# Kernel optimization log

Hardware: AMD Instinct MI355X
Metric: run time of the kernel (lower is better)

The kernel has to match this reference:

```python
import jax, jax.numpy as jnp
import numpy as np

B, T, N = 1024, 64, 128
E = 256          # embedding_size
H = 256          # hidden_size (== attention embed_dim)
NH = 256         # node_hidden_size (kdim/vdim)
HEADS = 4
DH = H // HEADS
F = 1            # edge_feature_len
L = 2            # gru layers


def setup_inputs() -> dict:
    key = jax.random.key(0)
    ks = iter(jax.random.split(key, 40))

    def rn(shape, s=0.05):
        return jax.random.normal(next(ks), shape, dtype=jnp.float32) * s

    z = lambda *shape: jnp.zeros(shape, jnp.float32)
    inp = {
        "x": rn((B, T, F), 1.0),
        "prev_node_hiddens": rn((B, N, NH), 1.0),
        # set_first_layer_hidden: layer 0 from GraphLevelRNN, layers > 0 zeroed
        "h0": jnp.concatenate([rn((1, B, H), 1.0), jnp.zeros((L - 1, B, H), jnp.float32)], axis=0),
        "W_in": rn((E, F)), "b_in": z(E),
        "gru_Wih0": rn((3 * H, E)), "gru_Whh0": rn((3 * H, H)),
        "gru_bih0": z(3 * H), "gru_bhh0": z(3 * H),
        "gru_Wih1": rn((3 * H, H)), "gru_Whh1": rn((3 * H, H)),
        "gru_bih1": z(3 * H), "gru_bhh1": z(3 * H),
        "Wq": rn((H, H)), "Wk": rn((H, NH)), "Wv": rn((H, NH)),
        "bq": z(H), "bk": z(H), "bv": z(H),
        "Wo": rn((H, H)), "bo": z(H),
        "Wc": rn((E, 2 * H)), "bc": z(E),
        "W1": rn((E, E)), "b1": z(E),
        "W2": rn((F, E)), "b2": z(F),
        "attn_mask": jnp.zeros((B, N), dtype=bool),
    }
    return inp


def _gru_cell(x, h, Wih, Whh, bih, bhh):
    # PyTorch GRU cell math
    gi = x @ Wih.T + bih
    gh = h @ Whh.T + bhh
    i_r, i_z, i_n = jnp.split(gi, 3, axis=-1)
    h_r, h_z, h_n = jnp.split(gh, 3, axis=-1)
    r = jax.nn.sigmoid(i_r + h_r)
    zg = jax.nn.sigmoid(i_z + h_z)
    n = jnp.tanh(i_n + r * h_n)
    return (1.0 - zg) * n + zg * h


def reference(x, prev_node_hiddens, h0, W_in, b_in,
              gru_Wih0, gru_Whh0, gru_bih0, gru_bhh0,
              gru_Wih1, gru_Whh1, gru_bih1, gru_bhh1,
              Wq, Wk, Wv, bq, bk, bv, Wo, bo,
              Wc, bc, W1, b1, W2, b2, attn_mask):
    emb = jax.nn.relu(x @ W_in.T + b_in)                       # [B,T,E]
    # K/V projections depend only on prev_node_hiddens; project once
    # (math identical to the per-step nn.MultiheadAttention call).
    k = (prev_node_hiddens @ Wk.T + bk).reshape(B, N, HEADS, DH)
    v = (prev_node_hiddens @ Wv.T + bv).reshape(B, N, HEADS, DH)
    scale = 1.0 / np.sqrt(DH).astype(np.float32)
    neg = jnp.asarray(-1e9, jnp.float32)
    mask = attn_mask[:, None, :]                               # [B,1,N]

    def step(carry, xt):
        h_prev0, h_prev1 = carry
        h0n = _gru_cell(xt, h_prev0, gru_Wih0, gru_Whh0, gru_bih0, gru_bhh0)
        h1n = _gru_cell(h0n, h_prev1, gru_Wih1, gru_Whh1, gru_bih1, gru_bhh1)
        # single-token query = last-layer hidden state
        q = ((h1n @ Wq.T + bq) * scale).reshape(B, HEADS, DH)
        scores = jnp.einsum('bhd,bnhd->bhn', q, k)             # [B,HEADS,N]
        scores = jnp.where(mask, neg, scores)
        a = jax.nn.softmax(scores, axis=-1)
        ctx = jnp.einsum('bhn,bnhd->bhd', a, v).reshape(B, H) @ Wo.T + bo
        comb = jax.nn.relu(jnp.concatenate([h1n, ctx], axis=-1) @ Wc.T + bc)
        out = jax.nn.relu(comb @ W1.T + b1) @ W2.T + b2        # [B,F]
        return (h0n, h1n), out

    _, outs = jax.lax.scan(step, (h0[0], h0[1]), jnp.swapaxes(emb, 0, 1))
    logits = jnp.swapaxes(outs, 0, 1)                          # [B,T,F]
    return jax.nn.sigmoid(logits)
```

## Files before the change

### kernel.cpp

```cpp
#include <hip/hip_runtime.h>
#include <hip/hip_bf16.h>
#include <cstddef>
#include <cstdint>


#define B_  1024
#define T_  64
#define N_  128

typedef __attribute__((ext_vector_type(8))) short s16x8;
typedef __attribute__((ext_vector_type(4))) float f32x4;

__device__ __forceinline__ unsigned short f2b(float f) {
  unsigned int u = __float_as_uint(f);
  u += 0x7FFFu + ((u >> 16) & 1u);
  return (unsigned short)(u >> 16);
}
__device__ __forceinline__ float b2f(unsigned short s){ return __uint_as_float(((unsigned int)s) << 16); }
__device__ __forceinline__ float sigmoidf_(float x){ return 1.0f / (1.0f + __expf(-x)); }
__device__ __forceinline__ float tanhf_(float x){
  float t = __expf(-2.0f * fabsf(x));
  float r = (1.0f - t) / (1.0f + t);
  return x >= 0.0f ? r : -r;
}
__device__ __forceinline__ void gld_lds16(const void* g, void* l) {
  __builtin_amdgcn_global_load_lds(
      (const __attribute__((address_space(1))) void*)g,
      (__attribute__((address_space(3))) void*)l, 16, 0, 0);
}
#define WAITV3 asm volatile("s_waitcnt vmcnt(3)" ::: "memory")
#define WAITV0 asm volatile("s_waitcnt vmcnt(0)" ::: "memory")

__global__ void cvt_bf16(const float* __restrict__ s, unsigned short* __restrict__ d, int n) {
  int i = blockIdx.x * blockDim.x + threadIdx.x;
  if (i < n) d[i] = f2b(s[i]);
}

#define LDA 264
#define LDB 40

__global__ __launch_bounds__(256) void kv_gemm(
    const float* __restrict__ phn,
    const float* __restrict__ Wk, const float* __restrict__ Wv,
    const float* __restrict__ bk, const float* __restrict__ bv,
    unsigned short* __restrict__ k_all, unsigned short* __restrict__ v_all)
{
  __shared__ __align__(16) unsigned short Alds[64 * LDA];
  __shared__ __align__(16) unsigned short Blds[256 * LDB];
  const int tid = threadIdx.x;
  const int m0 = blockIdx.x * 64;
  const int n0 = blockIdx.y * 256;
  #pragma unroll
  for (int p = 0; p < 16; ++p) {
    int q = p * 256 + tid;
    int row = q >> 6, kq = q & 63;
    float4 f = *(const float4*)&phn[(size_t)(m0 + row) * 256 + (size_t)kq * 4];
    ushort4 h; h.x = f2b(f.x); h.y = f2b(f.y); h.z = f2b(f.z); h.w = f2b(f.w);
    *(ushort4*)&Alds[row * LDA + kq * 4] = h;
  }
  const int wave = tid >> 6, lane = tid & 63;
  const int lr = lane & 15, lk = (lane >> 4) * 8;
  f32x4 acc[16];
  #pragma unroll
  for (int t = 0; t < 16; ++t) {
    int j = n0 + t * 16 + lr;
    float bz = (j < 256) ? bk[j] : bv[j - 256];
    acc[t][0] = bz; acc[t][1] = bz; acc[t][2] = bz; acc[t][3] = bz;
  }
  for (int kc = 0; kc < 8; ++kc) {
    __syncthreads();
    #pragma unroll
    for (int p = 0; p < 8; ++p) {
      int j = p * 32 + (tid >> 3);
      int jg = n0 + j;
      const float* wrow = (jg < 256) ? &Wk[(size_t)jg * 256] : &Wv[(size_t)(jg - 256) * 256];
      float4 f = *(const float4*)&wrow[kc * 32 + (tid & 7) * 4];
      ushort4 h; h.x = f2b(f.x); h.y = f2b(f.y); h.z = f2b(f.z); h.w = f2b(f.w);
      *(ushort4*)&Blds[j * LDB + (tid & 7) * 4] = h;
    }
    __syncthreads();
    s16x8 a = *(const s16x8*)&Alds[(wave * 16 + lr) * LDA + kc * 32 + lk];
    #pragma unroll
    for (int t = 0; t < 16; ++t) {
      s16x8 b = *(const s16x8*)&Blds[(t * 16 + lr) * LDB + lk];
      acc[t] = __builtin_amdgcn_mfma_f32_16x16x32_bf16(a, b, acc[t], 0, 0, 0);
    }
  }
  const int rbase = m0 + wave * 16 + (lane >> 4) * 4;
  #pragma unroll
  for (int t = 0; t < 16; ++t) {
    int j = n0 + t * 16 + lr;
    #pragma unroll
    for (int i = 0; i < 4; ++i) {
      size_t m = (size_t)(rbase + i);
      unsigned short hv = f2b(acc[t][i]);
      if (j < 256) k_all[m * 256 + j] = hv;
      else         v_all[m * 256 + (j - 256)] = hv;
    }
  }
}

__global__ __launch_bounds__(256) void gi0_gemm(
    const float* __restrict__ x, const float* __restrict__ W_in, const float* __restrict__ b_in,
    const float* __restrict__ Wih0, const float* __restrict__ bih0,
    unsigned short* __restrict__ gi0)
{
  __shared__ __align__(16) unsigned short Alds[64 * LDA];
  __shared__ __align__(16) unsigned short Blds[256 * LDB];
  const int tid = threadIdx.x;
  const int m0 = blockIdx.x * 64;
  const int f0 = blockIdx.y * 256;
  float win = W_in[tid], bin = b_in[tid];
  for (int p = 0; p < 64; ++p) {
    float e = fmaxf(fmaf(x[m0 + p], win, bin), 0.0f);
    Alds[p * LDA + tid] = f2b(e);
  }
  const int wave = tid >> 6, lane = tid & 63;
  const int lr = lane & 15, lk = (lane >> 4) * 8;
  f32x4 acc[16];
  #pragma unroll
  for (int t = 0; t < 16; ++t) {
    float bz = bih0[f0 + t * 16 + lr];
    acc[t][0] = bz; acc[t][1] = bz; acc[t][2] = bz; acc[t][3] = bz;
  }
  for (int kc = 0; kc < 8; ++kc) {
    __syncthreads();
    #pragma unroll
    for (int p = 0; p < 8; ++p) {
      int j = p * 32 + (tid >> 3);
      const float* wrow = &Wih0[(size_t)(f0 + j) * 256];
      float4 f = *(const float4*)&wrow[kc * 32 + (tid & 7) * 4];
      ushort4 h; h.x = f2b(f.x); h.y = f2b(f.y); h.z = f2b(f.z); h.w = f2b(f.w);
      *(ushort4*)&Blds[j * LDB + (tid & 7) * 4] = h;
    }
    __syncthreads();
    s16x8 a = *(const s16x8*)&Alds[(wave * 16 + lr) * LDA + kc * 32 + lk];
    #pragma unroll
    for (int t = 0; t < 16; ++t) {
      s16x8 b = *(const s16x8*)&Blds[(t * 16 + lr) * LDB + lk];
      acc[t] = __builtin_amdgcn_mfma_f32_16x16x32_bf16(a, b, acc[t], 0, 0, 0);
    }
  }
  const int rbase = m0 + wave * 16 + (lane >> 4) * 4;
  #pragma unroll
  for (int t = 0; t < 16; ++t) {
    int f = f0 + t * 16 + lr;
    #pragma unroll
    for (int i = 0; i < 4; ++i) {
      int m = rbase + i;
      gi0[((size_t)(m & 63) * 1024 + (m >> 6)) * 768 + f] = f2b(acc[t][i]);
    }
  }
}

__global__ __launch_bounds__(512) void seq2_kernel(
    const unsigned short* __restrict__ gi0,
    const float* __restrict__ h0_init,
    const unsigned short* __restrict__ w_hh0, const float* __restrict__ bhh0,
    const unsigned short* __restrict__ w_ih1, const float* __restrict__ bih1,
    const unsigned short* __restrict__ w_hh1, const float* __restrict__ bhh1,
    unsigned short* __restrict__ h1_all)
{
  __shared__ __align__(16) unsigned short wbuf[8][8][512];
  __shared__ __align__(16) float h0f[4][256];
  __shared__ __align__(16) float h1f[4][256];
  __shared__ __align__(16) unsigned short h0b[4][264];
  __shared__ __align__(16) unsigned short h1b[4][264];

  const int tid = threadIdx.x;
  const int w = tid >> 6, lane = tid & 63;
  const int col = lane & 15, kg = lane >> 4;
  const int b0 = blockIdx.x * 4;

  for (int i = tid; i < 1024; i += 512) {
    int g = i >> 8, f = i & 255;
    float v0 = h0_init[(size_t)(b0 + g) * 256 + f];
    float v1 = h0_init[(size_t)(B_ * 256) + (size_t)(b0 + g) * 256 + f];
    h0f[g][f] = v0; h1f[g][f] = v1;
    h0b[g][f] = f2b(v0); h1b[g][f] = f2b(v1);
  }
  __syncthreads();

  unsigned int off6[6];
  #pragma unroll
  for (int j = 0; j < 6; ++j) {
    int r0 = (j >> 1) * 256 + w * 32 + (j & 1) * 16;
    off6[j] = (unsigned)((r0 + col) * 256 + kg * 8);
  }
  float bb0[6], bb1[12];
  #pragma unroll
  for (int j = 0; j < 6; ++j) {
    int f = (j >> 1) * 256 + w * 32 + (j & 1) * 16 + col;
    bb0[j] = bhh0[f];
    bb1[j] = bih1[f];
    bb1[6 + j] = bhh1[f];
  }

  #pragma unroll 1
  for (int t = 0; t < T_; ++t) {
    f32x4 acc[6];
    #pragma unroll
    for (int j = 0; j < 6; ++j) { float bz = bb0[j]; acc[j][0]=bz; acc[j][1]=bz; acc[j][2]=bz; acc[j][3]=bz; }
    #pragma unroll
    for (int kc = 0; kc < 4; ++kc)
      gld_lds16(w_hh0 + off6[0] + kc * 32, &wbuf[w][kc][0]);
    #pragma unroll
    for (int j = 0; j < 6; ++j) {
      #pragma unroll
      for (int kc = 0; kc < 8; ++kc) {
        const int g = j * 8 + kc;
        if (g < 44) { WAITV3; } else if (g == 44) { WAITV0; }
        s16x8 bf_ = *(const s16x8*)&wbuf[w][g & 7][(size_t)lane * 8];
        s16x8 af_ = *(const s16x8*)&h0b[col & 3][kc * 32 + kg * 8];
        acc[j] = __builtin_amdgcn_mfma_f32_16x16x32_bf16(af_, bf_, acc[j], 0, 0, 0);
        if (g + 4 < 48) {
          const int gn = g + 4, jn = gn >> 3, kn = gn & 7;
          gld_lds16(w_hh0 + off6[jn] + kn * 32, &wbuf[w][gn & 7][0]);
        }
      }
    }
    if (lane < 16) {
      const size_t gbase = ((size_t)t * 1024 + b0) * 768;
      #pragma unroll
      for (int i = 0; i < 4; ++i) {
        const unsigned short* gp = gi0 + gbase + (size_t)i * 768;
        #pragma unroll
        for (int sub = 0; sub < 2; ++sub) {
          int f = w * 32 + sub * 16 + col;
          float ir = b2f(gp[f]), iz = b2f(gp[256 + f]), in_ = b2f(gp[512 + f]);
          float r = sigmoidf_(ir + acc[sub][i]);
          float z = sigmoidf_(iz + acc[2 + sub][i]);
          float n = tanhf_(in_ + r * acc[4 + sub][i]);
          float hn = (1.0f - z) * n + z * h0f[i][f];
          h0f[i][f] = hn;
          h0b[i][f] = f2b(hn);
        }
      }
    }
    __syncthreads();

    f32x4 acc2[12];
    #pragma unroll
    for (int j = 0; j < 12; ++j) { float bz = bb1[j]; acc2[j][0]=bz; acc2[j][1]=bz; acc2[j][2]=bz; acc2[j][3]=bz; }
    #pragma unroll
    for (int kc = 0; kc < 4; ++kc)
      gld_lds16(w_ih1 + off6[0] + kc * 32, &wbuf[w][kc][0]);
    #pragma unroll
    for (int j = 0; j < 12; ++j) {
      #pragma unroll
      for (int kc = 0; kc < 8; ++kc) {
        const int g = j * 8 + kc;
        if (g < 92) { WAITV3; } else if (g == 92) { WAITV0; }
        s16x8 bf_ = *(const s16x8*)&wbuf[w][g & 7][(size_t)lane * 8];
        s16x8 af_;
        if (j < 6) af_ = *(const s16x8*)&h0b[col & 3][kc * 32 + kg * 8];
        else       af_ = *(const s16x8*)&h1b[col & 3][kc * 32 + kg * 8];
        acc2[j] = __builtin_amdgcn_mfma_f32_16x16x32_bf16(af_, bf_, acc2[j], 0, 0, 0);
        if (g + 4 < 96) {
          const int gn = g + 4, jn = gn >> 3, kn = gn & 7;
          const unsigned short* wb = (jn < 6) ? w_ih1 : w_hh1;
          const unsigned int of = (jn < 6) ? off6[jn] : off6[jn - 6];
          gld_lds16(wb + of + kn * 32, &wbuf[w][gn & 7][0]);
        }
      }
    }
    if (lane < 16) {
      #pragma unroll
      for (int i = 0; i < 4; ++i) {
        #pragma unroll
        for (int sub = 0; sub < 2; ++sub) {
          int f = w * 32 + sub * 16 + col;
          float r = sigmoidf_(acc2[sub][i] + acc2[6 + sub][i]);
          float z = sigmoidf_(acc2[2 + sub][i] + acc2[8 + sub][i]);
          float n = tanhf_(acc2[4 + sub][i] + r * acc2[10 + sub][i]);
          float hn = (1.0f - z) * n + z * h1f[i][f];
          h1f[i][f] = hn;
          unsigned short hb = f2b(hn);
          h1b[i][f] = hb;
          h1_all[((size_t)(b0 + i) * T_ + t) * 256 + f] = hb;
        }
      }
    }
    __syncthreads();
  }
}

__global__ __launch_bounds__(256) void q_gemm(
    const unsigned short* __restrict__ h1_all,
    const unsigned short* __restrict__ w_q, const float* __restrict__ bq,
    unsigned short* __restrict__ q_all)
{
  __shared__ __align__(16) unsigned short A[64][264];
  const int tid = threadIdx.x;
  const int m0 = blockIdx.x * 64;
  #pragma unroll
  for (int p = 0; p < 8; ++p) {
    int idx = p * 256 + tid;
    int row = idx >> 5, c8 = idx & 31;
    *(uint4*)&A[row][c8 * 8] = *(const uint4*)&h1_all[(size_t)(m0 + row) * 256 + c8 * 8];
  }
  __syncthreads();
  const int wv = tid >> 6, lane = tid & 63;
  const int col = lane & 15, kg = lane >> 4;
  f32x4 acc[16];
  #pragma unroll
  for (int ct = 0; ct < 16; ++ct) {
    float bz = bq[ct * 16 + col];
    acc[ct][0]=bz; acc[ct][1]=bz; acc[ct][2]=bz; acc[ct][3]=bz;
  }
  #pragma unroll
  for (int kc = 0; kc < 8; ++kc) {
    s16x8 af = *(const s16x8*)&A[wv * 16 + col][kc * 32 + kg * 8];
    #pragma unroll
    for (int ct = 0; ct < 16; ++ct) {
      s16x8 bf = *(const s16x8*)&w_q[(size_t)(ct * 16 + col) * 256 + kc * 32 + kg * 8];
      acc[ct] = __builtin_amdgcn_mfma_f32_16x16x32_bf16(af, bf, acc[ct], 0, 0, 0);
    }
  }
  const int r0 = m0 + wv * 16 + kg * 4;
  #pragma unroll
  for (int ct = 0; ct < 16; ++ct) {
    int j = ct * 16 + col;
    #pragma unroll
    for (int i = 0; i < 4; ++i)
      q_all[(size_t)(r0 + i) * 256 + j] = f2b(acc[ct][i] * 0.125f);
  }
}

__global__ __launch_bounds__(256) void attn_kernel(
    const unsigned short* __restrict__ q_all,
    const unsigned short* __restrict__ k_all,
    const unsigned short* __restrict__ v_all,
    const unsigned char* __restrict__ amask,
    unsigned short* __restrict__ ctx_all)
{
  __shared__ __align__(16) unsigned short qh[64][72];
  __shared__ __align__(16) unsigned short kh[128][72];
  __shared__ __align__(16) unsigned short vT[64][136];
  __shared__ __align__(16) unsigned short P[64][136];
  const int b = blockIdx.x;
  const int tid = threadIdx.x;
  const int wv = tid >> 6, lane = tid & 63;
  const int col = lane & 15, kg = lane >> 4;
  bool mk[8];
  #pragma unroll
  for (int nt = 0; nt < 8; ++nt) mk[nt] = amask[(size_t)b * 128 + nt * 16 + col] != 0;

  #pragma unroll 1
  for (int h = 0; h < 4; ++h) {
    #pragma unroll
    for (int p = 0; p < 2; ++p) {
      int idx = p * 256 + tid, row = idx >> 3, c8 = idx & 7;
      *(uint4*)&qh[row][c8 * 8] = *(const uint4*)&q_all[((size_t)b * 64 + row) * 256 + h * 64 + c8 * 8];
    }
    #pragma unroll
    for (int p = 0; p < 4; ++p) {
      int idx = p * 256 + tid, row = idx >> 3, c8 = idx & 7;
      *(uint4*)&kh[row][c8 * 8] = *(const uint4*)&k_all[((size_t)b * 128 + row) * 256 + h * 64 + c8 * 8];
    }
    #pragma unroll
    for (int rep = 0; rep < 32; ++rep) {
      int e = rep * 256 + tid;
      int n = e >> 6, d = e & 63;
      vT[d][n] = v_all[((size_t)b * 128 + n) * 256 + h * 64 + d];
    }
    __syncthreads();

    s16x8 aq0 = *(const s16x8*)&qh[wv * 16 + col][kg * 8];
    s16x8 aq1 = *(const s16x8*)&qh[wv * 16 + col][32 + kg * 8];
    f32x4 s[8];
    #pragma unroll
    for (int nt = 0; nt < 8; ++nt) {
      f32x4 z = {0.f, 0.f, 0.f, 0.f};
      s16x8 bk0 = *(const s16x8*)&kh[nt * 16 + col][kg * 8];
      s16x8 bk1 = *(const s16x8*)&kh[nt * 16 + col][32 + kg * 8];
      z = __builtin_amdgcn_mfma_f32_16x16x32_bf16(aq0, bk0, z, 0, 0, 0);
      z = __builtin_amdgcn_mfma_f32_16x16x32_bf16(aq1, bk1, z, 0, 0, 0);
      s[nt] = z;
    }
    #pragma unroll
    for (int nt = 0; nt < 8; ++nt)
      if (mk[nt]) { s[nt][0] = -1e9f; s[nt][1] = -1e9f; s[nt][2] = -1e9f; s[nt][3] = -1e9f; }
    f32x4 mx = s[0];
    #pragma unroll
    for (int nt = 1; nt < 8; ++nt)
      #pragma unroll
      for (int i = 0; i < 4; ++i) mx[i] = fmaxf(mx[i], s[nt][i]);
    #pragma unroll
    for (int i = 0; i < 4; ++i) {
      float m = mx[i];
      m = fmaxf(m, __shfl_xor(m, 1)); m = fmaxf(m, __shfl_xor(m, 2));
      m = fmaxf(m, __shfl_xor(m, 4)); m = fmaxf(m, __shfl_xor(m, 8));
      mx[i] = m;
    }
    f32x4 sm = {0.f, 0.f, 0.f, 0.f};
    #pragma unroll
    for (int nt = 0; nt < 8; ++nt)
      #pragma unroll
      for (int i = 0; i < 4; ++i) { s[nt][i] = __expf(s[nt][i] - mx[i]); sm[i] += s[nt][i]; }
    #pragma unroll
    for (int i = 0; i < 4; ++i) {
      float t2 = sm[i];
      t2 += __shfl_xor(t2, 1); t2 += __shfl_xor(t2, 2);
      t2 += __shfl_xor(t2, 4); t2 += __shfl_xor(t2, 8);
      sm[i] = 1.0f / t2;
    }
    #pragma unroll
    for (int nt = 0; nt < 8; ++nt)
      #pragma unroll
      for (int i = 0; i < 4; ++i)
        P[wv * 16 + kg * 4 + i][nt * 16 + col] = f2b(s[nt][i] * sm[i]);
    __syncthreads();

    f32x4 c4[4];
    #pragma unroll
    for (int dt = 0; dt < 4; ++dt) { c4[dt][0]=0.f; c4[dt][1]=0.f; c4[dt][2]=0.f; c4[dt][3]=0.f; }
    #pragma unroll
    for (int kc = 0; kc < 4; ++kc) {
      s16x8 ap = *(const s16x8*)&P[wv * 16 + col][kc * 32 + kg * 8];
      #pragma unroll
      for (int dt = 0; dt < 4; ++dt) {
        s16x8 bv_ = *(const s16x8*)&vT[dt * 16 + col][kc * 32 + kg * 8];
        c4[dt] = __builtin_amdgcn_mfma_f32_16x16x32_bf16(ap, bv_, c4[dt], 0, 0, 0);
      }
    }
    #pragma unroll
    for (int dt = 0; dt < 4; ++dt) {
      int d = h * 64 + dt * 16 + col;
      #pragma unroll
      for (int i = 0; i < 4; ++i)
        ctx_all[((size_t)b * 64 + wv * 16 + kg * 4 + i) * 256 + d] = f2b(c4[dt][i]);
    }
    __syncthreads();
  }
}

__global__ __launch_bounds__(256) void out_chain(
    const unsigned short* __restrict__ h1_all,
    const unsigned short* __restrict__ ctx_all,
    const unsigned short* __restrict__ w_o, const float* __restrict__ bo,
    const unsigned short* __restrict__ w_c, const float* __restrict__ bc,
    const unsigned short* __restrict__ w_1, const float* __restrict__ b1,
    const float* __restrict__ W2, const float* __restrict__ b2,
    float* __restrict__ out)
{
  __shared__ __align__(16) unsigned short BufA[64][264];
  __shared__ __align__(16) unsigned short BufB[64][264];
  const int b = blockIdx.x;
  const int tid = threadIdx.x;
  const int wv = tid >> 6, lane = tid & 63;
  const int col = lane & 15, kg = lane >> 4;
  const size_t mbase = (size_t)b * 64;
  #pragma unroll
  for (int p = 0; p < 8; ++p) {
    int idx = p * 256 + tid, row = idx >> 5, c8 = idx & 31;
    *(uint4*)&BufA[row][c8 * 8] = *(const uint4*)&h1_all[(mbase + row) * 256 + c8 * 8];
    *(uint4*)&BufB[row][c8 * 8] = *(const uint4*)&ctx_all[(mbase + row) * 256 + c8 * 8];
  }
  __syncthreads();
  f32x4 acc[16];

  #pragma unroll
  for (int ct = 0; ct < 16; ++ct) { float bz = bo[ct*16+col]; acc[ct][0]=bz; acc[ct][1]=bz; acc[ct][2]=bz; acc[ct][3]=bz; }
  #pragma unroll
  for (int kc = 0; kc < 8; ++kc) {
    s16x8 af = *(const s16x8*)&BufB[wv * 16 + col][kc * 32 + kg * 8];
    #pragma unroll
    for (int ct = 0; ct < 16; ++ct) {
      s16x8 bf = *(const s16x8*)&w_o[(size_t)(ct * 16 + col) * 256 + kc * 32 + kg * 8];
      acc[ct] = __builtin_amdgcn_mfma_f32_16x16x32_bf16(af, bf, acc[ct], 0, 0, 0);
    }
  }
  __syncthreads();
  #pragma unroll
  for (int ct = 0; ct < 16; ++ct)
    #pragma unroll
    for (int i = 0; i < 4; ++i)
      BufB[wv * 16 + kg * 4 + i][ct * 16 + col] = f2b(acc[ct][i]);
  __syncthreads();

  #pragma unroll
  for (int ct = 0; ct < 16; ++ct) { float bz = bc[ct*16+col]; acc[ct][0]=bz; acc[ct][1]=bz; acc[ct][2]=bz; acc[ct][3]=bz; }
  #pragma unroll
  for (int kc = 0; kc < 16; ++kc) {
    s16x8 af;
    if (kc < 8) af = *(const s16x8*)&BufA[wv * 16 + col][kc * 32 + kg * 8];
    else        af = *(const s16x8*)&BufB[wv * 16 + col][(kc - 8) * 32 + kg * 8];
    #pragma unroll
    for (int ct = 0; ct < 16; ++ct) {
      s16x8 bf = *(const s16x8*)&w_c[(size_t)(ct * 16 + col) * 512 + kc * 32 + kg * 8];
      acc[ct] = __builtin_amdgcn_mfma_f32_16x16x32_bf16(af, bf, acc[ct], 0, 0, 0);
    }
  }
  __syncthreads();
  #pragma unroll
  for (int ct = 0; ct < 16; ++ct)
    #pragma unroll
    for (int i = 0; i < 4; ++i)
      BufB[wv * 16 + kg * 4 + i][ct * 16 + col] = f2b(fmaxf(acc[ct][i], 0.0f));
  __syncthreads();

  #pragma unroll
  for (int ct = 0; ct < 16; ++ct) { float bz = b1[ct*16+col]; acc[ct][0]=bz; acc[ct][1]=bz; acc[ct][2]=bz; acc[ct][3]=bz; }
  #pragma unroll
  for (int kc = 0; kc < 8; ++kc) {
    s16x8 af = *(const s16x8*)&BufB[wv * 16 + col][kc * 32 + kg * 8];
    #pragma unroll
    for (int ct = 0; ct < 16; ++ct) {
      s16x8 bf = *(const s16x8*)&w_1[(size_t)(ct * 16 + col) * 256 + kc * 32 + kg * 8];
      acc[ct] = __builtin_amdgcn_mfma_f32_16x16x32_bf16(af, bf, acc[ct], 0, 0, 0);
    }
  }
  __syncthreads();
  #pragma unroll
  for (int ct = 0; ct < 16; ++ct)
    #pragma unroll
    for (int i = 0; i < 4; ++i)
      BufA[wv * 16 + kg * 4 + i][ct * 16 + col] = f2b(fmaxf(acc[ct][i], 0.0f));
  __syncthreads();

  {
    int r = tid >> 2, qq = tid & 3;
    float a = 0.0f;
    #pragma unroll
    for (int i2 = 0; i2 < 64; ++i2) {
      int k = qq * 64 + i2;
      a += b2f(BufA[r][k]) * W2[k];
    }
    a += __shfl_xor(a, 1); a += __shfl_xor(a, 2);
    if (qq == 0) out[mbase + r] = sigmoidf_(a + b2[0]);
  }
}

extern "C" void kernel_launch(void* const* d_in, const int* in_sizes, int n_in,
                              void* d_out, int out_size, void* d_ws, size_t ws_size,
                              hipStream_t stream)
{
  (void)in_sizes; (void)n_in; (void)out_size;
  const float* x    = (const float*)d_in[0];
  const float* phn  = (const float*)d_in[1];
  const float* h0i  = (const float*)d_in[2];
  const float* W_in = (const float*)d_in[3];
  const float* b_in = (const float*)d_in[4];
  const float* Wih0 = (const float*)d_in[5];
  const float* Whh0 = (const float*)d_in[6];
  const float* bih0 = (const float*)d_in[7];
  const float* bhh0 = (const float*)d_in[8];
  const float* Wih1 = (const float*)d_in[9];
  const float* Whh1 = (const float*)d_in[10];
  const float* bih1 = (const float*)d_in[11];
  const float* bhh1 = (const float*)d_in[12];
  const float* Wq = (const float*)d_in[13];
  const float* Wk = (const float*)d_in[14];
  const float* Wv = (const float*)d_in[15];
  const float* bq = (const float*)d_in[16];
  const float* bk = (const float*)d_in[17];
  const float* bv = (const float*)d_in[18];
  const float* Wo = (const float*)d_in[19];
  const float* bo = (const float*)d_in[20];
  const float* Wc = (const float*)d_in[21];
  const float* bc = (const float*)d_in[22];
  const float* W1 = (const float*)d_in[23];
  const float* b1 = (const float*)d_in[24];
  const float* W2 = (const float*)d_in[25];
  const float* b2 = (const float*)d_in[26];
  const unsigned char* amask = (const unsigned char*)d_in[27];
  float* out = (float*)d_out;

  unsigned short* ws = (unsigned short*)d_ws;
  size_t off = 0;
  unsigned short* w_hh0 = ws + off; off += 196608;
  unsigned short* w_ih1 = ws + off; off += 196608;
  unsigned short* w_hh1 = ws + off; off += 196608;
  unsigned short* w_q   = ws + off; off += 65536;
  unsigned short* w_o   = ws + off; off += 65536;
  unsigned short* w_c   = ws + off; off += 131072;
  unsigned short* w_1   = ws + off; off += 65536;
  unsigned short* k_all = ws + off; off += (size_t)B_ * N_ * 256;
  unsigned short* v_all = ws + off; off += (size_t)B_ * N_ * 256;
  unsigned short* h1_all = ws + off; off += (size_t)B_ * T_ * 256;
  unsigned short* bigR  = ws + off; off += (size_t)B_ * T_ * 768;
  unsigned short* gi0   = bigR;
  unsigned short* q_all = bigR;
  unsigned short* ctx_all = bigR + (size_t)B_ * T_ * 256;
  if (ws_size < off * sizeof(unsigned short)) return;

  hipLaunchKernelGGL(cvt_bf16, dim3(384), dim3(512), 0, stream, Whh0, w_hh0, 196608);
  hipLaunchKernelGGL(cvt_bf16, dim3(384), dim3(512), 0, stream, Wih1, w_ih1, 196608);
  hipLaunchKernelGGL(cvt_bf16, dim3(384), dim3(512), 0, stream, Whh1, w_hh1, 196608);
  hipLaunchKernelGGL(cvt_bf16, dim3(128), dim3(512), 0, stream, Wq, w_q, 65536);
  hipLaunchKernelGGL(cvt_bf16, dim3(128), dim3(512), 0, stream, Wo, w_o, 65536);
  hipLaunchKernelGGL(cvt_bf16, dim3(256), dim3(512), 0, stream, Wc, w_c, 131072);
  hipLaunchKernelGGL(cvt_bf16, dim3(128), dim3(512), 0, stream, W1, w_1, 65536);

  hipLaunchKernelGGL(kv_gemm, dim3(2048, 2), dim3(256), 0, stream,
                     phn, Wk, Wv, bk, bv, k_all, v_all);
  hipLaunchKernelGGL(gi0_gemm, dim3(1024, 3), dim3(256), 0, stream,
                     x, W_in, b_in, Wih0, bih0, gi0);
  hipLaunchKernelGGL(seq2_kernel, dim3(256), dim3(512), 0, stream,
                     gi0, h0i, w_hh0, bhh0, w_ih1, bih1, w_hh1, bhh1, h1_all);
  hipLaunchKernelGGL(q_gemm, dim3(1024), dim3(256), 0, stream,
                     h1_all, w_q, bq, q_all);
  hipLaunchKernelGGL(attn_kernel, dim3(1024), dim3(256), 0, stream,
                     q_all, k_all, v_all, amask, ctx_all);
  hipLaunchKernelGGL(out_chain, dim3(1024), dim3(256), 0, stream,
                     h1_all, ctx_all, w_o, bo, w_c, bc, w_1, b1, W2, b2, out);
}
```

Baseline: 4.512 ms.

## Repack GRU weights into MFMA fragment order and batch 16 rows per block

Weights for the two recurrent GRU layers are pre-packed into per-wave, per-lane MFMA fragment order. The sequential kernel then streams them straight into registers with a software prefetch ring, replacing the LDS staging. Each block now handles 16 batch rows instead of 4, so every weight load feeds four times as many rows and all 16 MFMA rows do useful work. gi0 is async-loaded into LDS, hidden state stays in registers, and h1 is written back with vector stores. The grid shrinks to 64 blocks, which leaves most CUs idle and adds register pressure.

```diff
diff --git a/kernel.cpp b/kernel.cpp
--- a/kernel.cpp
+++ b/kernel.cpp
@@ -28,12 +28,32 @@
       (const __attribute__((address_space(1))) void*)g,
       (__attribute__((address_space(3))) void*)l, 16, 0, 0);
 }
-#define WAITV3 asm volatile("s_waitcnt vmcnt(3)" ::: "memory")
-#define WAITV0 asm volatile("s_waitcnt vmcnt(0)" ::: "memory")
 
 __global__ void cvt_bf16(const float* __restrict__ s, unsigned short* __restrict__ d, int n) {
   int i = blockIdx.x * blockDim.x + threadIdx.x;
   if (i < n) d[i] = f2b(s[i]);
+}
+
+__global__ void pack_w1(const float* __restrict__ Whh0, unsigned short* __restrict__ dst) {
+  int d = blockIdx.x * 256 + threadIdx.x;
+  int e = d & 7, l = (d >> 3) & 63, blk = d >> 9;
+  int kc = blk & 7, tj = blk >> 3;
+  int j = tj % 6, w = tj / 6;
+  int row = (j >> 1) * 256 + w * 32 + (j & 1) * 16 + (l & 15);
+  int colk = kc * 32 + (l >> 4) * 8 + e;
+  dst[d] = f2b(Whh0[(size_t)row * 256 + colk]);
+}
+__global__ void pack_w2(const float* __restrict__ Wih1, const float* __restrict__ Whh1,
+                        unsigned short* __restrict__ dst) {
+  int d = blockIdx.x * 256 + threadIdx.x;
+  int e = d & 7, l = (d >> 3) & 63, blk = d >> 9;
+  int kc = blk & 7, tj = blk >> 3;
+  int j = tj % 12, w = tj / 12;
+  int jj = (j < 6) ? j : j - 6;
+  int row = (jj >> 1) * 256 + w * 32 + (jj & 1) * 16 + (l & 15);
+  int colk = kc * 32 + (l >> 4) * 8 + e;
+  const float* src = (j < 6) ? Wih1 : Whh1;
+  dst[d] = f2b(src[(size_t)row * 256 + colk]);
 }
 
 #define LDA 264
@@ -153,40 +173,35 @@
   }
 }
 
-__global__ __launch_bounds__(512) void seq2_kernel(
+__global__ __launch_bounds__(512) void seq3_kernel(
     const unsigned short* __restrict__ gi0,
     const float* __restrict__ h0_init,
-    const unsigned short* __restrict__ w_hh0, const float* __restrict__ bhh0,
-    const unsigned short* __restrict__ w_ih1, const float* __restrict__ bih1,
-    const unsigned short* __restrict__ w_hh1, const float* __restrict__ bhh1,
+    const unsigned short* __restrict__ wpk1,
+    const float* __restrict__ bhh0,
+    const unsigned short* __restrict__ wpk2,
+    const float* __restrict__ bih1, const float* __restrict__ bhh1,
     unsigned short* __restrict__ h1_all)
 {
-  __shared__ __align__(16) unsigned short wbuf[8][8][512];
-  __shared__ __align__(16) float h0f[4][256];
-  __shared__ __align__(16) float h1f[4][256];
-  __shared__ __align__(16) unsigned short h0b[4][264];
-  __shared__ __align__(16) unsigned short h1b[4][264];
+  __shared__ __align__(16) unsigned short h0b[16][264];
+  __shared__ __align__(16) unsigned short h1b[16][264];
+  __shared__ __align__(16) unsigned short gi0s[16 * 768];
 
   const int tid = threadIdx.x;
   const int w = tid >> 6, lane = tid & 63;
   const int col = lane & 15, kg = lane >> 4;
-  const int b0 = blockIdx.x * 4;
-
-  for (int i = tid; i < 1024; i += 512) {
-    int g = i >> 8, f = i & 255;
-    float v0 = h0_init[(size_t)(b0 + g) * 256 + f];
-    float v1 = h0_init[(size_t)(B_ * 256) + (size_t)(b0 + g) * 256 + f];
-    h0f[g][f] = v0; h1f[g][f] = v1;
-    h0b[g][f] = f2b(v0); h1b[g][f] = f2b(v1);
-  }
-  __syncthreads();
-
-  unsigned int off6[6];
-  #pragma unroll
-  for (int j = 0; j < 6; ++j) {
-    int r0 = (j >> 1) * 256 + w * 32 + (j & 1) * 16;
-    off6[j] = (unsigned)((r0 + col) * 256 + kg * 8);
-  }
+  const int b0 = blockIdx.x * 16;
+
+  float hp0[8], hp1[8];
+  #pragma unroll
+  for (int sub = 0; sub < 2; ++sub)
+    #pragma unroll
+    for (int i = 0; i < 4; ++i) {
+      int bt = kg * 4 + i, fl = w * 32 + sub * 16 + col;
+      float v0 = h0_init[(size_t)(b0 + bt) * 256 + fl];
+      float v1 = h0_init[(size_t)(B_ * 256) + (size_t)(b0 + bt) * 256 + fl];
+      hp0[sub * 4 + i] = v0; hp1[sub * 4 + i] = v1;
+      h0b[bt][fl] = f2b(v0); h1b[bt][fl] = f2b(v1);
+    }
   float bb0[6], bb1[12];
   #pragma unroll
   for (int j = 0; j < 6; ++j) {
@@ -195,93 +210,105 @@
     bb1[j] = bih1[f];
     bb1[6 + j] = bhh1[f];
   }
+  __syncthreads();
+
+  const unsigned short* w1base = wpk1 + (size_t)w * 24576 + (size_t)lane * 8;
+  const unsigned short* w2base = wpk2 + (size_t)w * 49152 + (size_t)lane * 8;
+
+  s16x8 Wr[8];
 
   #pragma unroll 1
   for (int t = 0; t < T_; ++t) {
+    {
+      const unsigned short* gsrc = gi0 + ((size_t)t * 1024 + b0) * 768;
+      #pragma unroll
+      for (int c = 0; c < 3; ++c)
+        gld_lds16(gsrc + (size_t)(w * 3 + c) * 512 + (size_t)lane * 8,
+                  &gi0s[(w * 3 + c) * 512]);
+    }
+    __builtin_amdgcn_sched_barrier(0);
+    #pragma unroll
+    for (int p = 0; p < 6; ++p)
+      Wr[p] = *(const s16x8*)(w1base + (size_t)p * 512);
+    s16x8 h0o[8], h1o[8];
+    #pragma unroll
+    for (int kc = 0; kc < 8; ++kc) {
+      h0o[kc] = *(const s16x8*)&h0b[col][kc * 32 + kg * 8];
+      h1o[kc] = *(const s16x8*)&h1b[col][kc * 32 + kg * 8];
+    }
+    asm volatile("s_waitcnt vmcnt(6)" ::: "memory");
+    __syncthreads();
+
     f32x4 acc[6];
     #pragma unroll
     for (int j = 0; j < 6; ++j) { float bz = bb0[j]; acc[j][0]=bz; acc[j][1]=bz; acc[j][2]=bz; acc[j][3]=bz; }
-    #pragma unroll
-    for (int kc = 0; kc < 4; ++kc)
-      gld_lds16(w_hh0 + off6[0] + kc * 32, &wbuf[w][kc][0]);
     #pragma unroll
     for (int j = 0; j < 6; ++j) {
       #pragma unroll
       for (int kc = 0; kc < 8; ++kc) {
         const int g = j * 8 + kc;
-        if (g < 44) { WAITV3; } else if (g == 44) { WAITV0; }
-        s16x8 bf_ = *(const s16x8*)&wbuf[w][g & 7][(size_t)lane * 8];
-        s16x8 af_ = *(const s16x8*)&h0b[col & 3][kc * 32 + kg * 8];
-        acc[j] = __builtin_amdgcn_mfma_f32_16x16x32_bf16(af_, bf_, acc[j], 0, 0, 0);
-        if (g + 4 < 48) {
-          const int gn = g + 4, jn = gn >> 3, kn = gn & 7;
-          gld_lds16(w_hh0 + off6[jn] + kn * 32, &wbuf[w][gn & 7][0]);
-        }
+        if (g + 6 < 48) Wr[(g + 6) & 7] = *(const s16x8*)(w1base + (size_t)(g + 6) * 512);
+        else            Wr[(g + 6) & 7] = *(const s16x8*)(w2base + (size_t)(g + 6 - 48) * 512);
+        acc[j] = __builtin_amdgcn_mfma_f32_16x16x32_bf16(h0o[kc], Wr[g & 7], acc[j], 0, 0, 0);
       }
     }
-    if (lane < 16) {
-      const size_t gbase = ((size_t)t * 1024 + b0) * 768;
+    #pragma unroll
+    for (int sub = 0; sub < 2; ++sub) {
+      const int fl = w * 32 + sub * 16 + col;
       #pragma unroll
       for (int i = 0; i < 4; ++i) {
-        const unsigned short* gp = gi0 + gbase + (size_t)i * 768;
-        #pragma unroll
-        for (int sub = 0; sub < 2; ++sub) {
-          int f = w * 32 + sub * 16 + col;
-          float ir = b2f(gp[f]), iz = b2f(gp[256 + f]), in_ = b2f(gp[512 + f]);
-          float r = sigmoidf_(ir + acc[sub][i]);
-          float z = sigmoidf_(iz + acc[2 + sub][i]);
-          float n = tanhf_(in_ + r * acc[4 + sub][i]);
-          float hn = (1.0f - z) * n + z * h0f[i][f];
-          h0f[i][f] = hn;
-          h0b[i][f] = f2b(hn);
-        }
+        const int bt = kg * 4 + i;
+        float ir  = b2f(gi0s[bt * 768 + fl]);
+        float iz  = b2f(gi0s[bt * 768 + 256 + fl]);
+        float in_ = b2f(gi0s[bt * 768 + 512 + fl]);
+        float r = sigmoidf_(ir + acc[0 + sub][i]);
+        float z = sigmoidf_(iz + acc[2 + sub][i]);
+        float n = tanhf_(in_ + r * acc[4 + sub][i]);
+        float hn = (1.0f - z) * n + z * hp0[sub * 4 + i];
+        hp0[sub * 4 + i] = hn;
+        h0b[bt][fl] = f2b(hn);
       }
     }
     __syncthreads();
 
+    s16x8 h0n[8];
+    #pragma unroll
+    for (int kc = 0; kc < 8; ++kc)
+      h0n[kc] = *(const s16x8*)&h0b[col][kc * 32 + kg * 8];
     f32x4 acc2[12];
     #pragma unroll
     for (int j = 0; j < 12; ++j) { float bz = bb1[j]; acc2[j][0]=bz; acc2[j][1]=bz; acc2[j][2]=bz; acc2[j][3]=bz; }
-    #pragma unroll
-    for (int kc = 0; kc < 4; ++kc)
-      gld_lds16(w_ih1 + off6[0] + kc * 32, &wbuf[w][kc][0]);
     #pragma unroll
     for (int j = 0; j < 12; ++j) {
       #pragma unroll
       for (int kc = 0; kc < 8; ++kc) {
         const int g = j * 8 + kc;
-        if (g < 92) { WAITV3; } else if (g == 92) { WAITV0; }
-        s16x8 bf_ = *(const s16x8*)&wbuf[w][g & 7][(size_t)lane * 8];
-        s16x8 af_;
-        if (j < 6) af_ = *(const s16x8*)&h0b[col & 3][kc * 32 + kg * 8];
-        else       af_ = *(const s16x8*)&h1b[col & 3][kc * 32 + kg * 8];
-        acc2[j] = __builtin_amdgcn_mfma_f32_16x16x32_bf16(af_, bf_, acc2[j], 0, 0, 0);
-        if (g + 4 < 96) {
-          const int gn = g + 4, jn = gn >> 3, kn = gn & 7;
-          const unsigned short* wb = (jn < 6) ? w_ih1 : w_hh1;
-          const unsigned int of = (jn < 6) ? off6[jn] : off6[jn - 6];
-          gld_lds16(wb + of + kn * 32, &wbuf[w][gn & 7][0]);
-        }
+        if (g + 6 < 96) Wr[(g + 6) & 7] = *(const s16x8*)(w2base + (size_t)(g + 6) * 512);
+        s16x8 af = (j < 6) ? h0n[kc] : h1o[kc];
+        acc2[j] = __builtin_amdgcn_mfma_f32_16x16x32_bf16(af, Wr[g & 7], acc2[j], 0, 0, 0);
       }
     }
-    if (lane < 16) {
+    #pragma unroll
+    for (int sub = 0; sub < 2; ++sub) {
+      const int fl = w * 32 + sub * 16 + col;
       #pragma unroll
       for (int i = 0; i < 4; ++i) {
-        #pragma unroll
-        for (int sub = 0; sub < 2; ++sub) {
-          int f = w * 32 + sub * 16 + col;
-          float r = sigmoidf_(acc2[sub][i] + acc2[6 + sub][i]);
-          float z = sigmoidf_(acc2[2 + sub][i] + acc2[8 + sub][i]);
-          float n = tanhf_(acc2[4 + sub][i] + r * acc2[10 + sub][i]);
-          float hn = (1.0f - z) * n + z * h1f[i][f];
-          h1f[i][f] = hn;
-          unsigned short hb = f2b(hn);
-          h1b[i][f] = hb;
-          h1_all[((size_t)(b0 + i) * T_ + t) * 256 + f] = hb;
-        }
+        const int bt = kg * 4 + i;
+        float r = sigmoidf_(acc2[0 + sub][i] + acc2[6 + sub][i]);
+        float z = sigmoidf_(acc2[2 + sub][i] + acc2[8 + sub][i]);
+        float n = tanhf_(acc2[4 + sub][i] + r * acc2[10 + sub][i]);
+        float hn = (1.0f - z) * n + z * hp1[sub * 4 + i];
+        hp1[sub * 4 + i] = hn;
+        h1b[bt][fl] = f2b(hn);
       }
     }
     __syncthreads();
+
+    {
+      const int row = 2 * w + (lane >> 5), c16 = lane & 31;
+      s16x8 vv = *(const s16x8*)&h1b[row][c16 * 8];
+      *(s16x8*)&h1_all[((size_t)(b0 + row) * T_ + t) * 256 + c16 * 8] = vv;
+    }
   }
 }
 
@@ -569,9 +596,8 @@
 
   unsigned short* ws = (unsigned short*)d_ws;
   size_t off = 0;
-  unsigned short* w_hh0 = ws + off; off += 196608;
-  unsigned short* w_ih1 = ws + off; off += 196608;
-  unsigned short* w_hh1 = ws + off; off += 196608;
+  unsigned short* wpk1  = ws + off; off += 196608;
+  unsigned short* wpk2  = ws + off; off += 393216;
   unsigned short* w_q   = ws + off; off += 65536;
   unsigned short* w_o   = ws + off; off += 65536;
   unsigned short* w_c   = ws + off; off += 131072;
@@ -585,9 +611,8 @@
   unsigned short* ctx_all = bigR + (size_t)B_ * T_ * 256;
   if (ws_size < off * sizeof(unsigned short)) return;
 
-  hipLaunchKernelGGL(cvt_bf16, dim3(384), dim3(512), 0, stream, Whh0, w_hh0, 196608);
-  hipLaunchKernelGGL(cvt_bf16, dim3(384), dim3(512), 0, stream, Wih1, w_ih1, 196608);
-  hipLaunchKernelGGL(cvt_bf16, dim3(384), dim3(512), 0, stream, Whh1, w_hh1, 196608);
+  hipLaunchKernelGGL(pack_w1, dim3(768), dim3(256), 0, stream, Whh0, wpk1);
+  hipLaunchKernelGGL(pack_w2, dim3(1536), dim3(256), 0, stream, Wih1, Whh1, wpk2);
   hipLaunchKernelGGL(cvt_bf16, dim3(128), dim3(512), 0, stream, Wq, w_q, 65536);
   hipLaunchKernelGGL(cvt_bf16, dim3(128), dim3(512), 0, stream, Wo, w_o, 65536);
   hipLaunchKernelGGL(cvt_bf16, dim3(256), dim3(512), 0, stream, Wc, w_c, 131072);
@@ -597,8 +622,8 @@
                      phn, Wk, Wv, bk, bv, k_all, v_all);
   hipLaunchKernelGGL(gi0_gemm, dim3(1024, 3), dim3(256), 0, stream,
                      x, W_in, b_in, Wih0, bih0, gi0);
-  hipLaunchKernelGGL(seq2_kernel, dim3(256), dim3(512), 0, stream,
-                     gi0, h0i, w_hh0, bhh0, w_ih1, bih1, w_hh1, bhh1, h1_all);
+  hipLaunchKernelGGL(seq3_kernel, dim3(64), dim3(512), 0, stream,
+                     gi0, h0i, wpk1, bhh0, wpk2, bih1, bhh1, h1_all);
   hipLaunchKernelGGL(q_gemm, dim3(1024), dim3(256), 0, stream,
                      h1_all, w_q, bq, q_all);
   hipLaunchKernelGGL(attn_kernel, dim3(1024), dim3(256), 0, stream,
```

New measurement: 4.731 ms. +4.8%, slower.
